# Kernel optimization log

Hardware: AMD Instinct MI355X
Metric: run time of the kernel (lower is better)

## Reference

```python
import jax, jax.numpy as jnp
import numpy as np

COST_CLASS = 1.0
COST_BBOX = 5.0
COST_GIOU = 2.0
EPS = 1e-6

BS, Q, T = 8, 900, 256   # batch, num_queries, max_text_len
M = 2000                 # total target boxes concatenated over batch


def setup_inputs() -> dict:
    key = jax.random.key(0)
    k1, k2, k3, k4 = jax.random.split(key, 4)
    pred_logits = jax.random.normal(k1, (BS, Q, T), dtype=jnp.float32)
    pred_boxes = jax.random.uniform(k2, (BS, Q, 4), dtype=jnp.float32, minval=0.05, maxval=0.95)
    tgt_boxes = jax.random.uniform(k3, (M, 4), dtype=jnp.float32, minval=0.05, maxval=0.95)
    tgt_labels = jax.random.uniform(k4, (M, T), dtype=jnp.float32)  # positive token map (soft)
    return {"pred_logits": pred_logits, "pred_boxes": pred_boxes,
            "tgt_boxes": tgt_boxes, "tgt_labels": tgt_labels}


def box_cxcywh_to_xyxy(b):
    cx, cy, w, h = b[..., 0], b[..., 1], b[..., 2], b[..., 3]
    return jnp.stack([cx - 0.5 * w, cy - 0.5 * h, cx + 0.5 * w, cy + 0.5 * h], axis=-1)


def generalized_box_iou(boxes1, boxes2):
    # boxes1: [N,4] xyxy, boxes2: [M,4] xyxy -> [N,M] GIoU
    area1 = (boxes1[:, 2] - boxes1[:, 0]) * (boxes1[:, 3] - boxes1[:, 1])
    area2 = (boxes2[:, 2] - boxes2[:, 0]) * (boxes2[:, 3] - boxes2[:, 1])
    lt = jnp.maximum(boxes1[:, None, :2], boxes2[None, :, :2])  # [N,M,2]
    rb = jnp.minimum(boxes1[:, None, 2:], boxes2[None, :, 2:])
    wh = jnp.clip(rb - lt, 0.0)
    inter = wh[..., 0] * wh[..., 1]
    union = area1[:, None] + area2[None, :] - inter
    iou = inter / (union + EPS)
    lt_e = jnp.minimum(boxes1[:, None, :2], boxes2[None, :, :2])
    rb_e = jnp.maximum(boxes1[:, None, 2:], boxes2[None, :, 2:])
    wh_e = jnp.clip(rb_e - lt_e, 0.0)
    area_e = wh_e[..., 0] * wh_e[..., 1]
    return iou - (area_e - union) / (area_e + EPS)


def reference(pred_logits, pred_boxes, tgt_boxes, tgt_labels):
    bs, q, t = pred_logits.shape
    out_prob = jnp.clip(jax.nn.sigmoid(pred_logits.reshape(bs * q, t)), EPS, 1.0 - EPS)
    pred_bbox = pred_boxes.reshape(bs * q, 4)
    # normalized positive token map
    norm_labels = tgt_labels / (jnp.sum(tgt_labels, axis=1, keepdims=True) + EPS)
    # classification cost: -sum_t p[n,t] * map[m,t]  -> [N, M]
    cost_class = -jnp.einsum('nt,mt->nm', out_prob, norm_labels)
    # L1 box cost (cdist p=1) on cxcywh
    cost_bbox = jnp.sum(jnp.abs(pred_bbox[:, None, :] - tgt_boxes[None, :, :]), axis=-1)
    # GIoU cost on xyxy, clamped to >= -1
    giou = generalized_box_iou(box_cxcywh_to_xyxy(pred_bbox), box_cxcywh_to_xyxy(tgt_boxes))
    cost_giou = -jnp.clip(giou, -1.0)
    C = COST_BBOX * cost_bbox + COST_CLASS * cost_class + COST_GIOU * cost_giou
    return C.reshape(bs, q, -1)
```

## Files before the change

kernel.cpp:

```cpp
#include <hip/hip_runtime.h>
#include <math.h>

#define EPSF 1e-6f

typedef __attribute__((ext_vector_type(8))) short bf16x8;
typedef __attribute__((ext_vector_type(4))) float f32x4;
typedef __attribute__((ext_vector_type(4))) unsigned short u16x4;
typedef __attribute__((ext_vector_type(8))) unsigned short u16x8;

constexpr int TT = 256, MT = 2000, NP = 7200;

static __device__ __forceinline__ unsigned short f2bf(float f) {
    unsigned int u = __float_as_uint(f);
    u += 0x7FFFu + ((u >> 16) & 1u);
    return (unsigned short)(u >> 16);
}
static __device__ __forceinline__ float frcp(float x) { return __builtin_amdgcn_rcpf(x); }

__global__ __launch_bounds__(256) void prep_kernel(const float* __restrict__ logits,
                                                   const float* __restrict__ lab,
                                                   unsigned short* __restrict__ probs,
                                                   unsigned short* __restrict__ nlab) {
    int b = blockIdx.x;
    if (b < 900) {
        int i = (b * 256 + threadIdx.x) * 8;
        float4 x0 = *reinterpret_cast<const float4*>(logits + i);
        float4 x1 = *reinterpret_cast<const float4*>(logits + i + 4);
        float v[8] = {x0.x, x0.y, x0.z, x0.w, x1.x, x1.y, x1.z, x1.w};
        u16x8 o;
#pragma unroll
        for (int j = 0; j < 8; ++j) {
            float s = frcp(1.0f + __expf(-v[j]));
            s = fminf(fmaxf(s, EPSF), 1.0f - EPSF);
            o[j] = f2bf(s);
        }
        *reinterpret_cast<u16x8*>(probs + i) = o;
    } else {
        int wave = threadIdx.x >> 6;
        int lane = threadIdx.x & 63;
        int m = (b - 900) * 4 + wave;
        float4 v = reinterpret_cast<const float4*>(lab)[m * (TT / 4) + lane];
        float s = v.x + v.y + v.z + v.w;
#pragma unroll
        for (int off = 32; off > 0; off >>= 1) s += __shfl_down(s, off);
        float inv = frcp(__shfl(s, 0) + EPSF);
        u16x4 o;
        o[0] = f2bf(v.x * inv); o[1] = f2bf(v.y * inv);
        o[2] = f2bf(v.z * inv); o[3] = f2bf(v.w * inv);
        *reinterpret_cast<u16x4*>(nlab + m * TT + lane * 4) = o;
    }
}

constexpr int NTX = 113, NTY = 32;
constexpr int LDR = 132;

__global__ __launch_bounds__(256, 4) void cost_mfma_kernel(
    const unsigned short* __restrict__ A,
    const unsigned short* __restrict__ B,
    const float* __restrict__ pbox,
    const float* __restrict__ tbox,
    float* __restrict__ out)
{
    __shared__ __align__(16) unsigned short As[64 * LDR];
    __shared__ __align__(16) unsigned short Bs[64 * LDR];

    int n = blockIdx.x;
    int l = (n & 7) * 452 + (n >> 3);
    const int n0 = (l >> 5) * 64;
    const int m0 = (l & 31) * 64;

    const int tid = threadIdx.x;
    const int lane = tid & 63, wave = tid >> 6;
    const int wr = wave & 1, wc = wave >> 1;
    const int fr = lane & 15, quad = lane >> 4;

    const int s_row = tid >> 4;
    const int s_ch  = tid & 15;

    int gn4[4], gm4[4];
#pragma unroll
    for (int i = 0; i < 4; ++i) {
        int row = s_row + i * 16;
        int gn = n0 + row; gn4[i] = gn > NP - 1 ? NP - 1 : gn;
        int gm = m0 + row; gm4[i] = gm > MT - 1 ? MT - 1 : gm;
    }

    float4 tb[2]; int mj[2]; bool mv[2];
#pragma unroll
    for (int tj = 0; tj < 2; ++tj) {
        int gm = m0 + wc * 32 + tj * 16 + fr;
        mv[tj] = gm < MT; mj[tj] = gm;
        int g = mv[tj] ? gm : MT - 1;
        tb[tj] = *reinterpret_cast<const float4*>(&tbox[g * 4]);
    }
    float4 pbv[2][4]; int pr[2][4];
#pragma unroll
    for (int ti = 0; ti < 2; ++ti)
#pragma unroll
        for (int r = 0; r < 4; ++r) {
            int p = n0 + wr * 32 + ti * 16 + quad * 4 + r;
            pr[ti][r] = p;
            int g = p < NP ? p : NP - 1;
            pbv[ti][r] = *reinterpret_cast<const float4*>(&pbox[g * 4]);
        }

    bf16x8 sa[4], sb[4];
#pragma unroll
    for (int i = 0; i < 4; ++i) {
        sa[i] = *reinterpret_cast<const bf16x8*>(&A[gn4[i] * TT + s_ch * 8]);
        sb[i] = *reinterpret_cast<const bf16x8*>(&B[gm4[i] * TT + s_ch * 8]);
    }
#pragma unroll
    for (int i = 0; i < 4; ++i) {
        int row = s_row + i * 16;
        *reinterpret_cast<bf16x8*>(&As[row * LDR + s_ch * 8]) = sa[i];
        *reinterpret_cast<bf16x8*>(&Bs[row * LDR + s_ch * 8]) = sb[i];
    }
    __syncthreads();

    bf16x8 sa1[4], sb1[4];
#pragma unroll
    for (int i = 0; i < 4; ++i) {
        sa1[i] = *reinterpret_cast<const bf16x8*>(&A[gn4[i] * TT + 128 + s_ch * 8]);
        sb1[i] = *reinterpret_cast<const bf16x8*>(&B[gm4[i] * TT + 128 + s_ch * 8]);
    }

    f32x4 acc[2][2] = {};
#pragma unroll
    for (int kk = 0; kk < 4; ++kk) {
        bf16x8 af[2], bg[2];
#pragma unroll
        for (int t = 0; t < 2; ++t) {
            af[t] = *reinterpret_cast<const bf16x8*>(
                &As[(wr * 32 + t * 16 + fr) * LDR + kk * 32 + quad * 8]);
            bg[t] = *reinterpret_cast<const bf16x8*>(
                &Bs[(wc * 32 + t * 16 + fr) * LDR + kk * 32 + quad * 8]);
        }
#pragma unroll
        for (int ti = 0; ti < 2; ++ti)
#pragma unroll
            for (int tj = 0; tj < 2; ++tj)
                acc[ti][tj] = __builtin_amdgcn_mfma_f32_16x16x32_bf16(
                    af[ti], bg[tj], acc[ti][tj], 0, 0, 0);
    }
    __syncthreads();

#pragma unroll
    for (int i = 0; i < 4; ++i) {
        int row = s_row + i * 16;
        *reinterpret_cast<bf16x8*>(&As[row * LDR + s_ch * 8]) = sa1[i];
        *reinterpret_cast<bf16x8*>(&Bs[row * LDR + s_ch * 8]) = sb1[i];
    }
    __syncthreads();

#pragma unroll
    for (int kk = 0; kk < 4; ++kk) {
        bf16x8 af[2], bg[2];
#pragma unroll
        for (int t = 0; t < 2; ++t) {
            af[t] = *reinterpret_cast<const bf16x8*>(
                &As[(wr * 32 + t * 16 + fr) * LDR + kk * 32 + quad * 8]);
            bg[t] = *reinterpret_cast<const bf16x8*>(
                &Bs[(wc * 32 + t * 16 + fr) * LDR + kk * 32 + quad * 8]);
        }
#pragma unroll
        for (int ti = 0; ti < 2; ++ti)
#pragma unroll
            for (int tj = 0; tj < 2; ++tj)
                acc[ti][tj] = __builtin_amdgcn_mfma_f32_16x16x32_bf16(
                    af[ti], bg[tj], acc[ti][tj], 0, 0, 0);
    }

    float bcx[2], bcy[2], bww[2], bhh[2], bx1[2], by1[2], bx2[2], by2[2], areaB[2];
#pragma unroll
    for (int tj = 0; tj < 2; ++tj) {
        float4 b = tb[tj];
        bcx[tj] = b.x; bcy[tj] = b.y; bww[tj] = b.z; bhh[tj] = b.w;
        bx1[tj] = b.x - 0.5f * b.z; by1[tj] = b.y - 0.5f * b.w;
        bx2[tj] = b.x + 0.5f * b.z; by2[tj] = b.y + 0.5f * b.w;
        areaB[tj] = (bx2[tj] - bx1[tj]) * (by2[tj] - by1[tj]);
    }

#pragma unroll
    for (int ti = 0; ti < 2; ++ti) {
#pragma unroll
        for (int r = 0; r < 4; ++r) {
            int p = pr[ti][r];
            if (p >= NP) continue;
            float4 pb4 = pbv[ti][r];
            float ax1 = pb4.x - 0.5f * pb4.z, ay1 = pb4.y - 0.5f * pb4.w;
            float ax2 = pb4.x + 0.5f * pb4.z, ay2 = pb4.y + 0.5f * pb4.w;
            float areaA = (ax2 - ax1) * (ay2 - ay1);
#pragma unroll
            for (int tj = 0; tj < 2; ++tj) {
                if (!mv[tj]) continue;
                float l1 = fabsf(pb4.x - bcx[tj]) + fabsf(pb4.y - bcy[tj]) +
                           fabsf(pb4.z - bww[tj]) + fabsf(pb4.w - bhh[tj]);
                float ltx = fmaxf(ax1, bx1[tj]), lty = fmaxf(ay1, by1[tj]);
                float rbx = fminf(ax2, bx2[tj]), rby = fminf(ay2, by2[tj]);
                float iw = fmaxf(rbx - ltx, 0.0f), ih = fmaxf(rby - lty, 0.0f);
                float inter = iw * ih;
                float uni = areaA + areaB[tj] - inter;
                float iou = inter * frcp(uni + EPSF);
                float ex1 = fminf(ax1, bx1[tj]), ey1 = fminf(ay1, by1[tj]);
                float ex2 = fmaxf(ax2, bx2[tj]), ey2 = fmaxf(ay2, by2[tj]);
                float ew = fmaxf(ex2 - ex1, 0.0f), eh = fmaxf(ey2 - ey1, 0.0f);
                float areaE = ew * eh;
                float giou = iou - (areaE - uni) * frcp(areaE + EPSF);
                float res = 5.0f * l1 - acc[ti][tj][r] - 2.0f * fmaxf(giou, -1.0f);
                out[p * MT + mj[tj]] = res;
            }
        }
    }
}

extern "C" void kernel_launch(void* const* d_in, const int* in_sizes, int n_in,
                              void* d_out, int out_size, void* d_ws, size_t ws_size,
                              hipStream_t stream) {
    const float* pred_logits = (const float*)d_in[0];
    const float* pred_boxes  = (const float*)d_in[1];
    const float* tgt_boxes   = (const float*)d_in[2];
    const float* tgt_labels  = (const float*)d_in[3];
    float* out = (float*)d_out;

    unsigned short* probs = (unsigned short*)d_ws;
    unsigned short* nlab  = probs + NP * TT;

    prep_kernel<<<900 + 500, 256, 0, stream>>>(pred_logits, tgt_labels, probs, nlab);

    cost_mfma_kernel<<<NTX * NTY, 256, 0, stream>>>(probs, nlab, pred_boxes, tgt_boxes, out);
}
```

Before: 102.8 us.

## Load MFMA operands directly from global memory, dropping LDS staging

Removes the shared-memory staging of A and B tiles and the barriers around it. Each wave now reads its bf16 MFMA fragments straight from global memory (via L1/L2) across all 8 k-steps. Box loads move from the prologue into the epilogue, and the occupancy hint in the launch bounds is dropped. This saves LDS traffic and synchronisation, but each operand row is now fetched by several waves, so global and cache traffic rises and loads are less coalesced.

```diff
diff --git a/kernel.cpp b/kernel.cpp
--- a/kernel.cpp
+++ b/kernel.cpp
@@ -52,18 +52,14 @@
 }
 
 constexpr int NTX = 113, NTY = 32;
-constexpr int LDR = 132;
 
-__global__ __launch_bounds__(256, 4) void cost_mfma_kernel(
+__global__ __launch_bounds__(256) void cost_mfma_kernel(
     const unsigned short* __restrict__ A,
     const unsigned short* __restrict__ B,
     const float* __restrict__ pbox,
     const float* __restrict__ tbox,
     float* __restrict__ out)
 {
-    __shared__ __align__(16) unsigned short As[64 * LDR];
-    __shared__ __align__(16) unsigned short Bs[64 * LDR];
-
     int n = blockIdx.x;
     int l = (n & 7) * 452 + (n >> 3);
     const int n0 = (l >> 5) * 64;
@@ -74,94 +70,24 @@
     const int wr = wave & 1, wc = wave >> 1;
     const int fr = lane & 15, quad = lane >> 4;
 
-    const int s_row = tid >> 4;
-    const int s_ch  = tid & 15;
-
-    int gn4[4], gm4[4];
+    const unsigned short* ap[2];
+    const unsigned short* bp[2];
 #pragma unroll
-    for (int i = 0; i < 4; ++i) {
-        int row = s_row + i * 16;
-        int gn = n0 + row; gn4[i] = gn > NP - 1 ? NP - 1 : gn;
-        int gm = m0 + row; gm4[i] = gm > MT - 1 ? MT - 1 : gm;
-    }
-
-    float4 tb[2]; int mj[2]; bool mv[2];
-#pragma unroll
-    for (int tj = 0; tj < 2; ++tj) {
-        int gm = m0 + wc * 32 + tj * 16 + fr;
-        mv[tj] = gm < MT; mj[tj] = gm;
-        int g = mv[tj] ? gm : MT - 1;
-        tb[tj] = *reinterpret_cast<const float4*>(&tbox[g * 4]);
-    }
-    float4 pbv[2][4]; int pr[2][4];
-#pragma unroll
-    for (int ti = 0; ti < 2; ++ti)
-#pragma unroll
-        for (int r = 0; r < 4; ++r) {
-            int p = n0 + wr * 32 + ti * 16 + quad * 4 + r;
-            pr[ti][r] = p;
-            int g = p < NP ? p : NP - 1;
-            pbv[ti][r] = *reinterpret_cast<const float4*>(&pbox[g * 4]);
-        }
-
-    bf16x8 sa[4], sb[4];
-#pragma unroll
-    for (int i = 0; i < 4; ++i) {
-        sa[i] = *reinterpret_cast<const bf16x8*>(&A[gn4[i] * TT + s_ch * 8]);
-        sb[i] = *reinterpret_cast<const bf16x8*>(&B[gm4[i] * TT + s_ch * 8]);
-    }
-#pragma unroll
-    for (int i = 0; i < 4; ++i) {
-        int row = s_row + i * 16;
-        *reinterpret_cast<bf16x8*>(&As[row * LDR + s_ch * 8]) = sa[i];
-        *reinterpret_cast<bf16x8*>(&Bs[row * LDR + s_ch * 8]) = sb[i];
-    }
-    __syncthreads();
-
-    bf16x8 sa1[4], sb1[4];
-#pragma unroll
-    for (int i = 0; i < 4; ++i) {
-        sa1[i] = *reinterpret_cast<const bf16x8*>(&A[gn4[i] * TT + 128 + s_ch * 8]);
-        sb1[i] = *reinterpret_cast<const bf16x8*>(&B[gm4[i] * TT + 128 + s_ch * 8]);
+    for (int t = 0; t < 2; ++t) {
+        int ga = n0 + wr * 32 + t * 16 + fr; if (ga > NP - 1) ga = NP - 1;
+        int gb = m0 + wc * 32 + t * 16 + fr; if (gb > MT - 1) gb = MT - 1;
+        ap[t] = A + ga * TT + quad * 8;
+        bp[t] = B + gb * TT + quad * 8;
     }
 
     f32x4 acc[2][2] = {};
 #pragma unroll
-    for (int kk = 0; kk < 4; ++kk) {
+    for (int kk = 0; kk < 8; ++kk) {
         bf16x8 af[2], bg[2];
 #pragma unroll
         for (int t = 0; t < 2; ++t) {
-            af[t] = *reinterpret_cast<const bf16x8*>(
-                &As[(wr * 32 + t * 16 + fr) * LDR + kk * 32 + quad * 8]);
-            bg[t] = *reinterpret_cast<const bf16x8*>(
-                &Bs[(wc * 32 + t * 16 + fr) * LDR + kk * 32 + quad * 8]);
-        }
-#pragma unroll
-        for (int ti = 0; ti < 2; ++ti)
-#pragma unroll
-            for (int tj = 0; tj < 2; ++tj)
-                acc[ti][tj] = __builtin_amdgcn_mfma_f32_16x16x32_bf16(
-                    af[ti], bg[tj], acc[ti][tj], 0, 0, 0);
-    }
-    __syncthreads();
-
-#pragma unroll
-    for (int i = 0; i < 4; ++i) {
-        int row = s_row + i * 16;
-        *reinterpret_cast<bf16x8*>(&As[row * LDR + s_ch * 8]) = sa1[i];
-        *reinterpret_cast<bf16x8*>(&Bs[row * LDR + s_ch * 8]) = sb1[i];
-    }
-    __syncthreads();
-
-#pragma unroll
-    for (int kk = 0; kk < 4; ++kk) {
-        bf16x8 af[2], bg[2];
-#pragma unroll
-        for (int t = 0; t < 2; ++t) {
-            af[t] = *reinterpret_cast<const bf16x8*>(
-                &As[(wr * 32 + t * 16 + fr) * LDR + kk * 32 + quad * 8]);
-            bg[t] = *reinterpret_cast<const bf16x8*>(
-                &Bs[(wc * 32 + t * 16 + fr) * LDR + kk * 32 + quad * 8]);
+            af[t] = *reinterpret_cast<const bf16x8*>(ap[t] + kk * 32);
+            bg[t] = *reinterpret_cast<const bf16x8*>(bp[t] + kk * 32);
         }
 #pragma unroll
         for (int ti = 0; ti < 2; ++ti)
@@ -172,9 +98,13 @@
     }
 
     float bcx[2], bcy[2], bww[2], bhh[2], bx1[2], by1[2], bx2[2], by2[2], areaB[2];
+    int mj[2]; bool mv[2];
 #pragma unroll
     for (int tj = 0; tj < 2; ++tj) {
-        float4 b = tb[tj];
+        int gm = m0 + wc * 32 + tj * 16 + fr;
+        mv[tj] = gm < MT; mj[tj] = gm;
+        int g = mv[tj] ? gm : MT - 1;
+        float4 b = *reinterpret_cast<const float4*>(&tbox[g * 4]);
         bcx[tj] = b.x; bcy[tj] = b.y; bww[tj] = b.z; bhh[tj] = b.w;
         bx1[tj] = b.x - 0.5f * b.z; by1[tj] = b.y - 0.5f * b.w;
         bx2[tj] = b.x + 0.5f * b.z; by2[tj] = b.y + 0.5f * b.w;
@@ -185,9 +115,9 @@
     for (int ti = 0; ti < 2; ++ti) {
 #pragma unroll
         for (int r = 0; r < 4; ++r) {
-            int p = pr[ti][r];
+            int p = n0 + wr * 32 + ti * 16 + quad * 4 + r;
             if (p >= NP) continue;
-            float4 pb4 = pbv[ti][r];
+            float4 pb4 = *reinterpret_cast<const float4*>(&pbox[p * 4]);
             float ax1 = pb4.x - 0.5f * pb4.z, ay1 = pb4.y - 0.5f * pb4.w;
             float ax2 = pb4.x + 0.5f * pb4.z, ay2 = pb4.y + 0.5f * pb4.w;
             float areaA = (ax2 - ax1) * (ay2 - ay1);
```

Measured after the change: 140.1 us. 36.2% more time.

## Transpose MFMA operand roles to emit vectorized float4 output stores

Applied to the files above, without the earlier changes.

Swaps the A and B operands of the MFMA so each lane's four accumulator registers map to four consecutive target columns of one prediction row. The epilogue can then write one 16-byte vector store per 4 outputs instead of four scattered scalar stores. It also folds the two GIoU reciprocals into one and drops the enclosing-box clamp. The cost is loading four target boxes per lane. Because MT=2000 is divisible by 4, every 4-column group lies entirely inside or outside range, so the aligned vector store stays in bounds.

```diff
diff --git a/kernel.cpp b/kernel.cpp
--- a/kernel.cpp
+++ b/kernel.cpp
@@ -85,24 +85,24 @@
         int gm = m0 + row; gm4[i] = gm > MT - 1 ? MT - 1 : gm;
     }
 
-    float4 tb[2]; int mj[2]; bool mv[2];
-#pragma unroll
-    for (int tj = 0; tj < 2; ++tj) {
-        int gm = m0 + wc * 32 + tj * 16 + fr;
-        mv[tj] = gm < MT; mj[tj] = gm;
-        int g = mv[tj] ? gm : MT - 1;
-        tb[tj] = *reinterpret_cast<const float4*>(&tbox[g * 4]);
-    }
-    float4 pbv[2][4]; int pr[2][4];
-#pragma unroll
-    for (int ti = 0; ti < 2; ++ti)
+    float4 tbv[2][4]; int mrow[2];
+#pragma unroll
+    for (int tm = 0; tm < 2; ++tm) {
+        mrow[tm] = m0 + wc * 32 + tm * 16 + quad * 4;
 #pragma unroll
         for (int r = 0; r < 4; ++r) {
-            int p = n0 + wr * 32 + ti * 16 + quad * 4 + r;
-            pr[ti][r] = p;
-            int g = p < NP ? p : NP - 1;
-            pbv[ti][r] = *reinterpret_cast<const float4*>(&pbox[g * 4]);
-        }
+            int g = mrow[tm] + r; g = g < MT ? g : MT - 1;
+            tbv[tm][r] = *reinterpret_cast<const float4*>(&tbox[g * 4]);
+        }
+    }
+    float4 pbv[2]; int prow[2];
+#pragma unroll
+    for (int tp = 0; tp < 2; ++tp) {
+        int p = n0 + wr * 32 + tp * 16 + fr;
+        prow[tp] = p;
+        int g = p < NP ? p : NP - 1;
+        pbv[tp] = *reinterpret_cast<const float4*>(&pbox[g * 4]);
+    }
 
     bf16x8 sa[4], sb[4];
 #pragma unroll
@@ -137,11 +137,11 @@
                 &Bs[(wc * 32 + t * 16 + fr) * LDR + kk * 32 + quad * 8]);
         }
 #pragma unroll
-        for (int ti = 0; ti < 2; ++ti)
-#pragma unroll
-            for (int tj = 0; tj < 2; ++tj)
-                acc[ti][tj] = __builtin_amdgcn_mfma_f32_16x16x32_bf16(
-                    af[ti], bg[tj], acc[ti][tj], 0, 0, 0);
+        for (int tm = 0; tm < 2; ++tm)
+#pragma unroll
+            for (int tp = 0; tp < 2; ++tp)
+                acc[tm][tp] = __builtin_amdgcn_mfma_f32_16x16x32_bf16(
+                    bg[tm], af[tp], acc[tm][tp], 0, 0, 0);
     }
     __syncthreads();
 
@@ -164,52 +164,49 @@
                 &Bs[(wc * 32 + t * 16 + fr) * LDR + kk * 32 + quad * 8]);
         }
 #pragma unroll
-        for (int ti = 0; ti < 2; ++ti)
-#pragma unroll
-            for (int tj = 0; tj < 2; ++tj)
-                acc[ti][tj] = __builtin_amdgcn_mfma_f32_16x16x32_bf16(
-                    af[ti], bg[tj], acc[ti][tj], 0, 0, 0);
-    }
-
-    float bcx[2], bcy[2], bww[2], bhh[2], bx1[2], by1[2], bx2[2], by2[2], areaB[2];
-#pragma unroll
-    for (int tj = 0; tj < 2; ++tj) {
-        float4 b = tb[tj];
-        bcx[tj] = b.x; bcy[tj] = b.y; bww[tj] = b.z; bhh[tj] = b.w;
-        bx1[tj] = b.x - 0.5f * b.z; by1[tj] = b.y - 0.5f * b.w;
-        bx2[tj] = b.x + 0.5f * b.z; by2[tj] = b.y + 0.5f * b.w;
-        areaB[tj] = (bx2[tj] - bx1[tj]) * (by2[tj] - by1[tj]);
-    }
-
-#pragma unroll
-    for (int ti = 0; ti < 2; ++ti) {
-#pragma unroll
-        for (int r = 0; r < 4; ++r) {
-            int p = pr[ti][r];
-            if (p >= NP) continue;
-            float4 pb4 = pbv[ti][r];
-            float ax1 = pb4.x - 0.5f * pb4.z, ay1 = pb4.y - 0.5f * pb4.w;
-            float ax2 = pb4.x + 0.5f * pb4.z, ay2 = pb4.y + 0.5f * pb4.w;
-            float areaA = (ax2 - ax1) * (ay2 - ay1);
-#pragma unroll
-            for (int tj = 0; tj < 2; ++tj) {
-                if (!mv[tj]) continue;
-                float l1 = fabsf(pb4.x - bcx[tj]) + fabsf(pb4.y - bcy[tj]) +
-                           fabsf(pb4.z - bww[tj]) + fabsf(pb4.w - bhh[tj]);
-                float ltx = fmaxf(ax1, bx1[tj]), lty = fmaxf(ay1, by1[tj]);
-                float rbx = fminf(ax2, bx2[tj]), rby = fminf(ay2, by2[tj]);
+        for (int tm = 0; tm < 2; ++tm)
+#pragma unroll
+            for (int tp = 0; tp < 2; ++tp)
+                acc[tm][tp] = __builtin_amdgcn_mfma_f32_16x16x32_bf16(
+                    bg[tm], af[tp], acc[tm][tp], 0, 0, 0);
+    }
+
+#pragma unroll
+    for (int tp = 0; tp < 2; ++tp) {
+        int p = prow[tp];
+        if (p >= NP) continue;
+        float4 pb = pbv[tp];
+        float ax1 = pb.x - 0.5f * pb.z, ay1 = pb.y - 0.5f * pb.w;
+        float ax2 = pb.x + 0.5f * pb.z, ay2 = pb.y + 0.5f * pb.w;
+        float areaA = pb.z * pb.w;
+        float* orow = out + (size_t)p * MT;
+#pragma unroll
+        for (int tm = 0; tm < 2; ++tm) {
+            int mb = mrow[tm];
+            if (mb >= MT) continue;
+            f32x4 res;
+#pragma unroll
+            for (int r = 0; r < 4; ++r) {
+                float4 b = tbv[tm][r];
+                float bx1 = b.x - 0.5f * b.z, by1 = b.y - 0.5f * b.w;
+                float bx2 = b.x + 0.5f * b.z, by2 = b.y + 0.5f * b.w;
+                float areaB = b.z * b.w;
+                float l1 = fabsf(pb.x - b.x) + fabsf(pb.y - b.y) +
+                           fabsf(pb.z - b.z) + fabsf(pb.w - b.w);
+                float ltx = fmaxf(ax1, bx1), lty = fmaxf(ay1, by1);
+                float rbx = fminf(ax2, bx2), rby = fminf(ay2, by2);
                 float iw = fmaxf(rbx - ltx, 0.0f), ih = fmaxf(rby - lty, 0.0f);
                 float inter = iw * ih;
-                float uni = areaA + areaB[tj] - inter;
-                float iou = inter * frcp(uni + EPSF);
-                float ex1 = fminf(ax1, bx1[tj]), ey1 = fminf(ay1, by1[tj]);
-                float ex2 = fmaxf(ax2, bx2[tj]), ey2 = fmaxf(ay2, by2[tj]);
-                float ew = fmaxf(ex2 - ex1, 0.0f), eh = fmaxf(ey2 - ey1, 0.0f);
-                float areaE = ew * eh;
-                float giou = iou - (areaE - uni) * frcp(areaE + EPSF);
-                float res = 5.0f * l1 - acc[ti][tj][r] - 2.0f * fmaxf(giou, -1.0f);
-                out[p * MT + mj[tj]] = res;
+                float uni = areaA + areaB - inter;
+                float ex1 = fminf(ax1, bx1), ey1 = fminf(ay1, by1);
+                float ex2 = fmaxf(ax2, bx2), ey2 = fmaxf(ay2, by2);
+                float areaE = (ex2 - ex1) * (ey2 - ey1);
+                float ue = uni + EPSF, ae = areaE + EPSF;
+                float g = (inter * ae - (areaE - uni) * ue) * frcp(ue * ae);
+                res[r] = fmaf(-2.0f, fmaxf(g, -1.0f),
+                              fmaf(5.0f, l1, -acc[tm][tp][r]));
             }
+            *reinterpret_cast<f32x4*>(orow + mb) = res;
         }
     }
 }
```

Measured after the change: 105.9 us. +3.0%, slower.
